# Optimization experiments

Hardware: AMD Instinct MI355X
Metric: run time of the kernel (lower is better)

Reference implementation:

```python
import jax, jax.numpy as jnp
import numpy as np

DIM = 1024
HEADS = 16
DIM_HEAD = 64
INNER = HEADS * DIM_HEAD  # 1024
EPS = 1e-5


def layernorm(x, w, b):
    mu = jnp.mean(x, axis=-1, keepdims=True)
    var = jnp.mean(jnp.square(x - mu), axis=-1, keepdims=True)
    return (x - mu) * jax.lax.rsqrt(var + EPS) * w + b


def setup_inputs() -> dict:
    key = jax.random.key(0)
    ks = jax.random.split(key, 9)
    b, n1, n2 = 4, 4096, 256
    x = jax.random.normal(ks[0], (b, n1, DIM), dtype=jnp.float32)
    latents = jax.random.normal(ks[1], (b, n2, DIM), dtype=jnp.float32)
    shift = jax.random.normal(ks[2], (b, HEADS), dtype=jnp.float32)
    scale = jax.random.normal(ks[3], (b, HEADS), dtype=jnp.float32)
    s = 1.0 / np.sqrt(DIM)
    Wq = jax.random.normal(ks[4], (DIM, INNER), dtype=jnp.float32) * s
    Wkv = jax.random.normal(ks[5], (DIM, 2 * INNER), dtype=jnp.float32) * s
    Wout = jax.random.normal(ks[6], (INNER, DIM), dtype=jnp.float32) * (1.0 / np.sqrt(INNER))
    ln1_w = jnp.ones((DIM,), jnp.float32)
    ln1_b = jnp.zeros((DIM,), jnp.float32)
    ln2_w = jnp.ones((DIM,), jnp.float32)
    ln2_b = jnp.zeros((DIM,), jnp.float32)
    return {"x": x, "latents": latents, "shift": shift, "scale": scale,
            "ln1_w": ln1_w, "ln1_b": ln1_b, "ln2_w": ln2_w, "ln2_b": ln2_b,
            "Wq": Wq, "Wkv": Wkv, "Wout": Wout}


def reference(x, latents, shift, scale, ln1_w, ln1_b, ln2_w, ln2_b, Wq, Wkv, Wout):
    b = x.shape[0]
    xn = layernorm(x, ln1_w, ln1_b)            # (b, n1, D)
    ln = layernorm(latents, ln2_w, ln2_b)      # (b, n2, D)
    q = ln @ Wq                                 # (b, n2, inner)
    kv = xn @ Wkv                               # (b, n1, 2*inner)
    k, v = jnp.split(kv, 2, axis=-1)
    q = q.reshape(b, -1, HEADS, DIM_HEAD)
    k = k.reshape(b, -1, HEADS, DIM_HEAD)
    v = v.reshape(b, -1, HEADS, DIM_HEAD)
    # AdaLN-style per-head modulation on q
    q = q * (1.0 + scale[:, None, :, None]) + shift[:, None, :, None]
    # fp32 attention scores (already fp32 here)
    attn_scale = DIM_HEAD ** -0.5
    qk = jnp.einsum('bihd,bjhd->bhij', q.astype(jnp.float32), k.astype(jnp.float32)) * attn_scale
    attn = jax.nn.softmax(qk, axis=-1).astype(v.dtype)  # (b, h, n2, n1)
    out = jnp.einsum('bhij,bjhd->bihd', attn, v)         # (b, n2, h, dh)
    out = out.reshape(b, -1, INNER)
    return out @ Wout
```

## Files before the change

### kernel.cpp

```cpp
#include <hip/hip_runtime.h>

typedef __bf16 bf16;
typedef bf16 bf16x8 __attribute__((ext_vector_type(8)));
typedef bf16 bf16x4 __attribute__((ext_vector_type(4)));
typedef float f32x4 __attribute__((ext_vector_type(4)));

#define B_ 4
#define N1 4096
#define N2 256
#define DIM 1024
#define HEADS 16
#define DH 64
#define INNER 1024
#define ASPLIT 4
#define KEYS_PER_SPLIT (N1 / ASPLIT)
#define SPLIT_ELEMS (4 * 16 * 256 * 64)
#define ROWS_TOTAL (4 * HEADS * N2)

typedef __attribute__((address_space(1))) const void gvoid_t;
typedef __attribute__((address_space(3))) void lvoid_t;
__device__ __forceinline__ void async16(const void* g, void* l) {
  __builtin_amdgcn_global_load_lds((gvoid_t*)g, (lvoid_t*)l, 16, 0, 0);
}

__global__ __launch_bounds__(256) void prep(
    const float* __restrict__ Wq, const float* __restrict__ Wkv,
    const float* __restrict__ Wout, bf16* __restrict__ WqT,
    bf16* __restrict__ WkvT, bf16* __restrict__ WoutT,
    const float* __restrict__ x, const float* __restrict__ latents,
    const float* __restrict__ ln1w, const float* __restrict__ ln1b,
    const float* __restrict__ ln2w, const float* __restrict__ ln2b,
    bf16* __restrict__ xn, bf16* __restrict__ lnl) {
  __shared__ float tile[32][33];
  int t = blockIdx.x;
  if (t < 4096) {
    const float* src;
    bf16* dst;
    int N;
    if (t < 1024) { src = Wq; dst = WqT; N = 1024; }
    else if (t < 3072) { t -= 1024; src = Wkv; dst = WkvT; N = 2048; }
    else { t -= 3072; src = Wout; dst = WoutT; N = 1024; }
    int ntiles = N >> 5;
    int n0 = (t % ntiles) * 32, k0 = (t / ntiles) * 32;
    int xx = threadIdx.x & 31, yy = threadIdx.x >> 5;
    for (int j = 0; j < 4; j++)
      tile[yy + 8 * j][xx] = src[(size_t)(k0 + yy + 8 * j) * N + n0 + xx];
    __syncthreads();
    for (int j = 0; j < 4; j++)
      dst[(size_t)(n0 + yy + 8 * j) * 1024 + k0 + xx] = (bf16)tile[xx][yy + 8 * j];
    return;
  }
  int wv = threadIdx.x >> 6, lane = threadIdx.x & 63;
  int grow = (t - 4096) * 4 + wv;
  const float *src, *w, *bb;
  bf16* dst;
  int row;
  if (grow < 16384) { src = x; w = ln1w; bb = ln1b; dst = xn; row = grow; }
  else { src = latents; w = ln2w; bb = ln2b; dst = lnl; row = grow - 16384; }
  const float4* p = (const float4*)(src + (size_t)row * DIM);
  float4 v[4];
  for (int j = 0; j < 4; j++) v[j] = p[j * 64 + lane];
  float s = 0.f, sq = 0.f;
  for (int j = 0; j < 4; j++) {
    s += v[j].x + v[j].y + v[j].z + v[j].w;
    sq += v[j].x * v[j].x + v[j].y * v[j].y + v[j].z * v[j].z + v[j].w * v[j].w;
  }
  for (int off = 32; off; off >>= 1) {
    s += __shfl_xor(s, off, 64);
    sq += __shfl_xor(sq, off, 64);
  }
  float mu = s * (1.0f / DIM);
  float var = sq * (1.0f / DIM) - mu * mu;
  float r = rsqrtf(var + 1e-5f);
  for (int j = 0; j < 4; j++) {
    float4 wv4 = ((const float4*)w)[j * 64 + lane];
    float4 bv4 = ((const float4*)bb)[j * 64 + lane];
    bf16x4 o;
    o[0] = (bf16)((v[j].x - mu) * r * wv4.x + bv4.x);
    o[1] = (bf16)((v[j].y - mu) * r * wv4.y + bv4.y);
    o[2] = (bf16)((v[j].z - mu) * r * wv4.z + bv4.z);
    o[3] = (bf16)((v[j].w - mu) * r * wv4.w + bv4.w);
    *(bf16x4*)(dst + (size_t)row * DIM + (j * 64 + lane) * 4) = o;
  }
}

__global__ __launch_bounds__(256) void gemm_kv(
    const bf16* __restrict__ A, const bf16* __restrict__ Bt,
    bf16* __restrict__ Cout, bf16* __restrict__ Cout2, int K) {
  __shared__ __align__(16) bf16 smem[128 * 64 * 2];
  bf16* As = smem;
  bf16* Bs = smem + 128 * 64;
  int tid = threadIdx.x;
  int lane = tid & 63, wv = tid >> 6;
  int wr = wv >> 1, wc = wv & 1;
  int quad = lane >> 4, lr = lane & 15;
  int bid = blockIdx.y * 16 + blockIdx.x;
  int c = bid & 7, g = bid >> 3;
  int mi = g & 7, nb = (g >> 3) & 15, chunk = g >> 7;
  int m0 = (chunk * 64 + mi * 8 + c) * 128;
  int n0 = nb * 128;
  f32x4 acc[4][4] = {};
  for (int kt = 0; kt < K; kt += 64) {
    __syncthreads();
    for (int j = 0; j < 4; j++) {
      int idx0 = j * 256 + wv * 64;
      int row = (idx0 >> 3) + (lane >> 3);
      int cb = (lane & 7) ^ (row & 7);
      async16(&A[(size_t)(m0 + row) * K + kt + cb * 8], &As[idx0 * 8]);
      async16(&Bt[(size_t)(n0 + row) * K + kt + cb * 8], &Bs[idx0 * 8]);
    }
    __syncthreads();
    for (int kk = 0; kk < 2; kk++) {
      bf16x8 af[4], bfr[4];
      for (int im = 0; im < 4; im++) {
        int row = wr * 64 + im * 16 + lr;
        af[im] = *(const bf16x8*)&As[row * 64 + ((quad + 4 * kk) ^ (row & 7)) * 8];
      }
      for (int in = 0; in < 4; in++) {
        int row = wc * 64 + in * 16 + lr;
        bfr[in] = *(const bf16x8*)&Bs[row * 64 + ((quad + 4 * kk) ^ (row & 7)) * 8];
      }
      for (int im = 0; im < 4; im++)
        for (int in = 0; in < 4; in++)
          acc[im][in] = __builtin_amdgcn_mfma_f32_16x16x32_bf16(
              af[im], bfr[in], acc[im][in], 0, 0, 0);
    }
  }

  if (n0 >= 1024) {
    bf16* Ct = smem;
    for (int pass = 0; pass < 2; pass++) {
      __syncthreads();
      for (int inL = 0; inL < 2; inL++) {
        int in = pass * 2 + inL;
        int cc = wc * 32 + inL * 16 + lr;
        for (int im = 0; im < 4; im++) {
          int rb = wr * 64 + im * 16 + quad * 4;
          bf16x4 pk;
          for (int r = 0; r < 4; r++) pk[r] = (bf16)acc[im][in][r];
          *(bf16x4*)&Ct[cc * 136 + rb] = pk;
        }
      }
      __syncthreads();
      for (int k2 = 0; k2 < 4; k2++) {
        int ci = k2 * 256 + tid;
        int cc = ci >> 4, ch = ci & 15;
        uint4 val = *(const uint4*)&Ct[cc * 136 + ch * 8];
        int gco = (cc >> 5) * 64 + pass * 32 + (cc & 31);
        int col = n0 - 1024 + gco;
        int bb2 = m0 >> 12;
        int key = (m0 & 4095) + ch * 8;
        *(uint4*)&Cout2[((size_t)(bb2 * 1024 + col)) * 4096 + key] = val;
      }
    }
    return;
  }

  for (int im = 0; im < 4; im++)
    for (int in = 0; in < 4; in++) {
      int col = n0 + wc * 64 + in * 16 + lr;
      for (int r = 0; r < 4; r++) {
        int row = m0 + wr * 64 + im * 16 + quad * 4 + r;
        Cout[(size_t)row * 1024 + col] = (bf16)acc[im][in][r];
      }
    }
}

template <int MODE>
__global__ __launch_bounds__(256) void gemm64(
    const bf16* __restrict__ A, const bf16* __restrict__ Bt,
    void* __restrict__ Cout, int K, int N,
    const float* __restrict__ shiftp, const float* __restrict__ scalep) {
  __shared__ __align__(16) bf16 As[64 * 64];
  __shared__ __align__(16) bf16 Bs[64 * 64];
  int tid = threadIdx.x;
  int lane = tid & 63, wv = tid >> 6;
  int wr = wv >> 1, wc = wv & 1;
  int quad = lane >> 4, lr = lane & 15;
  int m0 = blockIdx.y * 64, n0 = blockIdx.x * 64;
  f32x4 acc[2][2] = {};
  for (int kt = 0; kt < K; kt += 64) {
    __syncthreads();
    for (int j = 0; j < 2; j++) {
      int idx0 = j * 256 + wv * 64;
      int row = (idx0 >> 3) + (lane >> 3);
      int cb = (lane & 7) ^ (row & 7);
      async16(&A[(size_t)(m0 + row) * K + kt + cb * 8], &As[idx0 * 8]);
      async16(&Bt[(size_t)(n0 + row) * K + kt + cb * 8], &Bs[idx0 * 8]);
    }
    __syncthreads();
    for (int kk = 0; kk < 2; kk++) {
      bf16x8 af[2], bfr[2];
      for (int im = 0; im < 2; im++) {
        int row = wr * 32 + im * 16 + lr;
        af[im] = *(const bf16x8*)&As[row * 64 + ((quad + 4 * kk) ^ (row & 7)) * 8];
      }
      for (int in = 0; in < 2; in++) {
        int row = wc * 32 + in * 16 + lr;
        bfr[in] = *(const bf16x8*)&Bs[row * 64 + ((quad + 4 * kk) ^ (row & 7)) * 8];
      }
      for (int im = 0; im < 2; im++)
        for (int in = 0; in < 2; in++)
          acc[im][in] = __builtin_amdgcn_mfma_f32_16x16x32_bf16(
              af[im], bfr[in], acc[im][in], 0, 0, 0);
    }
  }
  for (int im = 0; im < 2; im++)
    for (int in = 0; in < 2; in++) {
      int col = n0 + wc * 32 + in * 16 + lr;
      for (int r = 0; r < 4; r++) {
        int row = m0 + wr * 32 + im * 16 + quad * 4 + r;
        float v = acc[im][in][r];
        if (MODE == 1) {
          int bb = row >> 8, hh = col >> 6;
          float sc = scalep[bb * 16 + hh], sh = shiftp[bb * 16 + hh];
          ((bf16*)Cout)[(size_t)row * N + col] =
              (bf16)((v * (1.0f + sc) + sh) * 0.18033688011112042f);
        } else {
          ((float*)Cout)[(size_t)row * N + col] = v;
        }
      }
    }
}

__global__ __launch_bounds__(256) void attn_kernel(const bf16* __restrict__ q,
                                                   const bf16* __restrict__ kb,
                                                   const bf16* __restrict__ vt,
                                                   bf16* __restrict__ opb,
                                                   float* __restrict__ lseb) {
  int b = blockIdx.z, h = blockIdx.y;
  int qp = blockIdx.x >> 2, sp = blockIdx.x & 3;
  int tid = threadIdx.x, lane = tid & 63, wv = tid >> 6;
  int quad = lane >> 4, lr = lane & 15;
  __shared__ __align__(16) bf16 Ks[64 * 64];
  __shared__ __align__(16) bf16 Vs[64 * 64];
  __shared__ __align__(16) bf16 QP[128 * 64];
  __shared__ float abuf[4][16];
  int q0 = qp * 128;

  const bf16* qg = q + (size_t)(b * N2 + q0) * INNER + h * DH;
  for (int j = 0; j < 4; j++) {
    int r0 = j * 32 + wv * 8;
    int r = r0 + (lane >> 3);
    async16(&qg[(size_t)r * INNER + ((lane & 7) ^ (r & 7)) * 8], &QP[r0 * 64]);
  }
  __syncthreads();
  bf16x8 aQ[2][2];
  for (int g = 0; g < 2; g++) {
    int row = wv * 32 + g * 16 + lr;
    for (int kk = 0; kk < 2; kk++)
      aQ[g][kk] = *(const bf16x8*)&QP[row * 64 + ((quad + 4 * kk) ^ (row & 7)) * 8];
  }
  float m_s[2] = {-1e30f, -1e30f}, l_s[2] = {0.0f, 0.0f};
  f32x4 oacc[2][4] = {};

  const bf16* kg = kb + (size_t)(b * N1) * 1024 + h * DH;
  const bf16* vg = vt + (size_t)((b * HEADS + h) * DH) * N1;
  bf16* Ps = QP + wv * 2048;

  for (int t = 0; t < KEYS_PER_SPLIT / 64; t++) {
    int key0 = sp * KEYS_PER_SPLIT + t * 64;
    __syncthreads();
    for (int j = 0; j < 2; j++) {
      int r0 = j * 32 + wv * 8;
      int r = r0 + (lane >> 3);
      int cs = ((lane & 7) ^ (r & 7)) * 8;
      async16(&kg[(size_t)(key0 + r) * 1024 + cs], &Ks[r0 * 64]);
      async16(&vg[(size_t)r * N1 + key0 + cs], &Vs[r0 * 64]);
    }
    __syncthreads();

    bf16x8 ak[2][4], bv[2][4];
    for (int kk = 0; kk < 2; kk++)
      for (int nt = 0; nt < 4; nt++) {
        int row = nt * 16 + lr;
        ak[kk][nt] =
            *(const bf16x8*)&Ks[row * 64 + ((quad + 4 * kk) ^ (row & 7)) * 8];
        bv[kk][nt] =
            *(const bf16x8*)&Vs[row * 64 + ((quad + 4 * kk) ^ (row & 7)) * 8];
      }

    for (int g = 0; g < 2; g++) {
      f32x4 s[4] = {};
      for (int kk = 0; kk < 2; kk++)
        for (int nt = 0; nt < 4; nt++)
          s[nt] = __builtin_amdgcn_mfma_f32_16x16x32_bf16(ak[kk][nt], aQ[g][kk],
                                                          s[nt], 0, 0, 0);
      float mx = s[0][0];
      for (int nt = 0; nt < 4; nt++)
        for (int r = 0; r < 4; r++) mx = fmaxf(mx, s[nt][r]);
      mx = fmaxf(mx, __shfl_xor(mx, 16, 64));
      mx = fmaxf(mx, __shfl_xor(mx, 32, 64));
      float mn = fmaxf(m_s[g], mx);
      float al = exp2f(m_s[g] - mn);
      float p[4][4], sum = 0.0f;
      for (int nt = 0; nt < 4; nt++)
        for (int r = 0; r < 4; r++) {
          p[nt][r] = exp2f(s[nt][r] - mn);
          sum += p[nt][r];
        }
      sum += __shfl_xor(sum, 16, 64);
      sum += __shfl_xor(sum, 32, 64);
      l_s[g] = l_s[g] * al + sum;
      m_s[g] = mn;
      if (quad == 0) abuf[wv][lr] = al;

      for (int nt = 0; nt < 4; nt++) {
        bf16x4 pk;
        for (int r = 0; r < 4; r++) pk[r] = (bf16)p[nt][r];
        *(bf16x4*)&Ps[lr * 64 + ((2 * nt + (quad >> 1)) ^ (lr & 7)) * 8 +
                      (quad & 1) * 4] = pk;
      }

      f32x4 a4 = *(const f32x4*)&abuf[wv][quad * 4];
      for (int in = 0; in < 4; in++)
        for (int r = 0; r < 4; r++) oacc[g][in][r] *= a4[r];

      bf16x8 aP[2];
      for (int kk = 0; kk < 2; kk++)
        aP[kk] = *(const bf16x8*)&Ps[lr * 64 + ((4 * kk + quad) ^ (lr & 7)) * 8];
      for (int kk = 0; kk < 2; kk++)
        for (int in = 0; in < 4; in++)
          oacc[g][in] = __builtin_amdgcn_mfma_f32_16x16x32_bf16(
              aP[kk], bv[kk][in], oacc[g][in], 0, 0, 0);
    }
  }

  bf16* ob = opb + (size_t)sp * SPLIT_ELEMS;
  size_t rbase = (size_t)(b * HEADS + h) * N2;
  for (int g = 0; g < 2; g++) {
    for (int r = 0; r < 4; r++) {
      float lrow = __shfl(l_s[g], quad * 4 + r, 16);
      float inv = 1.0f / lrow;
      int qq = q0 + wv * 32 + g * 16 + quad * 4 + r;
      for (int in = 0; in < 4; in++)
        ob[(rbase + qq) * 64 + in * 16 + lr] = (bf16)(oacc[g][in][r] * inv);
    }
    if (quad == 0) {
      int qq = q0 + wv * 32 + g * 16 + lr;
      lseb[(size_t)sp * ROWS_TOTAL + rbase + qq] = m_s[g] + __log2f(l_s[g]);
    }
  }
}

__global__ __launch_bounds__(256) void combine_kernel(const bf16* __restrict__ opb,
                                                      const float* __restrict__ lseb,
                                                      bf16* __restrict__ out) {
  int gid = blockIdx.x * 256 + threadIdx.x;
  int d = gid & 63;
  int rq = gid >> 6;
  int qq = rq & 255, bh = rq >> 8;
  int h = bh & 15, b = bh >> 4;
  float ls[ASPLIT];
  for (int s = 0; s < ASPLIT; s++) ls[s] = lseb[(size_t)s * ROWS_TOTAL + rq];
  float M = fmaxf(fmaxf(ls[0], ls[1]), fmaxf(ls[2], ls[3]));
  float L = 0.0f, o = 0.0f;
  for (int s = 0; s < ASPLIT; s++) {
    float w = exp2f(ls[s] - M);
    L += w;
    o += w * (float)opb[(size_t)s * SPLIT_ELEMS + (size_t)rq * 64 + d];
  }
  out[((size_t)(b * N2 + qq)) * INNER + h * DH + d] = (bf16)(o / L);
}

extern "C" void kernel_launch(void* const* d_in, const int* in_sizes, int n_in,
                              void* d_out, int out_size, void* d_ws,
                              size_t ws_size, hipStream_t stream) {
  const float* x       = (const float*)d_in[0];
  const float* latents = (const float*)d_in[1];
  const float* shift   = (const float*)d_in[2];
  const float* scale   = (const float*)d_in[3];
  const float* ln1w    = (const float*)d_in[4];
  const float* ln1b    = (const float*)d_in[5];
  const float* ln2w    = (const float*)d_in[6];
  const float* ln2b    = (const float*)d_in[7];
  const float* Wq      = (const float*)d_in[8];
  const float* Wkv     = (const float*)d_in[9];
  const float* Wout    = (const float*)d_in[10];

  char* ws = (char*)d_ws;
  bf16*  xn    = (bf16*)(ws);
  bf16*  opb   = (bf16*)(ws);
  bf16*  lnl   = (bf16*)(ws + 33554432);
  float* lseb  = (float*)(ws + 33554432);
  bf16*  qb    = (bf16*)(ws + 35651584);
  bf16*  kb    = (bf16*)(ws + 37748736);
  bf16*  vtb   = (bf16*)(ws + 104857600);
  bf16*  aob   = (bf16*)(ws + 138412032);
  bf16*  WqT   = (bf16*)(ws + 140509184);
  bf16*  WkvT  = (bf16*)(ws + 142606336);
  bf16*  WoutT = (bf16*)(ws + 146800640);

  prep<<<8448, 256, 0, stream>>>(Wq, Wkv, Wout, WqT, WkvT, WoutT, x, latents,
                                 ln1w, ln1b, ln2w, ln2b, xn, lnl);
  gemm_kv<<<dim3(16, 128), 256, 0, stream>>>(xn, WkvT, kb, vtb, 1024);
  gemm64<1><<<dim3(16, 16), 256, 0, stream>>>(lnl, WqT, qb, 1024, 1024, shift,
                                              scale);
  attn_kernel<<<dim3(2 * ASPLIT, 16, 4), 256, 0, stream>>>(qb, kb, vtb, opb,
                                                           lseb);
  combine_kernel<<<16384, 256, 0, stream>>>(opb, lseb, aob);
  gemm64<2><<<dim3(16, 16), 256, 0, stream>>>(aob, WoutT, d_out, 1024, 1024,
                                              nullptr, nullptr);
}
```

Measured before the change: 285.4 us.

## Rewrite KV GEMM with 256x256 tiles, double-buffered async LDS pipeline

```diff
diff --git a/kernel.cpp b/kernel.cpp
--- a/kernel.cpp
+++ b/kernel.cpp
@@ -84,86 +84,173 @@
   }
 }
 
-__global__ __launch_bounds__(256) void gemm_kv(
+__device__ __forceinline__ int swz_off(int row, int cb) {
+  int line = row >> 1;
+  return (line << 7) + (((((row & 1) << 2) | cb) ^ (line & 7)) << 4);
+}
+
+__global__ __launch_bounds__(512, 2) void gemm_kv256(
     const bf16* __restrict__ A, const bf16* __restrict__ Bt,
-    bf16* __restrict__ Cout, bf16* __restrict__ Cout2, int K) {
-  __shared__ __align__(16) bf16 smem[128 * 64 * 2];
-  bf16* As = smem;
-  bf16* Bs = smem + 128 * 64;
+    bf16* __restrict__ Cout, bf16* __restrict__ Cout2) {
+  extern __shared__ char smem[];
   int tid = threadIdx.x;
   int lane = tid & 63, wv = tid >> 6;
-  int wr = wv >> 1, wc = wv & 1;
-  int quad = lane >> 4, lr = lane & 15;
-  int bid = blockIdx.y * 16 + blockIdx.x;
-  int c = bid & 7, g = bid >> 3;
-  int mi = g & 7, nb = (g >> 3) & 15, chunk = g >> 7;
-  int m0 = (chunk * 64 + mi * 8 + c) * 128;
-  int n0 = nb * 128;
-  f32x4 acc[4][4] = {};
-  for (int kt = 0; kt < K; kt += 64) {
-    __syncthreads();
-    for (int j = 0; j < 4; j++) {
-      int idx0 = j * 256 + wv * 64;
-      int row = (idx0 >> 3) + (lane >> 3);
-      int cb = (lane & 7) ^ (row & 7);
-      async16(&A[(size_t)(m0 + row) * K + kt + cb * 8], &As[idx0 * 8]);
-      async16(&Bt[(size_t)(n0 + row) * K + kt + cb * 8], &Bs[idx0 * 8]);
-    }
-    __syncthreads();
-    for (int kk = 0; kk < 2; kk++) {
-      bf16x8 af[4], bfr[4];
-      for (int im = 0; im < 4; im++) {
-        int row = wr * 64 + im * 16 + lr;
-        af[im] = *(const bf16x8*)&As[row * 64 + ((quad + 4 * kk) ^ (row & 7)) * 8];
-      }
+  int lr = lane & 15, quad = lane >> 4;
+  int wr = wv >> 2, wc = wv & 3;
+  int bid = blockIdx.x;
+  int mt = (bid & 7) * 8 + ((bid >> 3) >> 3), nt = (bid >> 3) & 7;
+  int m0 = mt * 256, n0 = nt * 256;
+
+  int offA[8], offB[4];
+#pragma unroll
+  for (int im = 0; im < 8; im++) offA[im] = swz_off(wr * 128 + im * 16 + lr, quad);
+#pragma unroll
+  for (int in = 0; in < 4; in++) offB[in] = swz_off(wc * 64 + in * 16 + lr, quad);
+
+  size_t gA[2], gB[2];
+#pragma unroll
+  for (int s = 0; s < 2; s++) {
+    int u = s * 512 + tid;
+    int line = u >> 3, inner = (u & 7) ^ (line & 7);
+    int row = line * 2 + (inner >> 2), cb = inner & 3;
+    gA[s] = (size_t)(m0 + row) * 1024 + cb * 8;
+    gB[s] = (size_t)(n0 + row) * 1024 + cb * 8;
+  }
+  int ldsS0 = wv * 1024, ldsS1 = 8192 + wv * 1024;
+
+  auto stA = [&](int b, int kh, int k0) {
+    char* base = smem + b * 32768 + kh * 16384;
+    async16(&A[gA[0] + k0], base + ldsS0);
+    async16(&A[gA[1] + k0], base + ldsS1);
+  };
+  auto stB = [&](int b, int kh, int k0) {
+    char* base = smem + 65536 + b * 32768 + kh * 16384;
+    async16(&Bt[gB[0] + k0], base + ldsS0);
+    async16(&Bt[gB[1] + k0], base + ldsS1);
+  };
+
+  f32x4 acc[8][4] = {};
+
+  stA(0, 0, 0);  stB(0, 0, 0);
+  stA(0, 1, 32); stB(0, 1, 32);
+  stA(1, 0, 64); stB(1, 0, 64);
+  asm volatile("s_waitcnt vmcnt(4)" ::: "memory");
+  __builtin_amdgcn_s_barrier();
+
+#pragma unroll 1
+  for (int t = 0; t < 16; t++) {
+    int b = t & 1;
+    const char* A0 = smem + b * 32768;
+    const char* A1 = A0 + 16384;
+    const char* B0 = smem + 65536 + b * 32768;
+    const char* B1 = B0 + 16384;
+    int k1 = (t + 1 < 16 ? t + 1 : 15) * 64;
+    int k2 = (t + 2 < 16 ? t + 2 : 15) * 64;
+    bf16x8 af[4], bfr[4];
+#pragma unroll
+    for (int in = 0; in < 4; in++) bfr[in] = *(const bf16x8*)(B0 + offB[in]);
+#pragma unroll
+    for (int im = 0; im < 4; im++) af[im] = *(const bf16x8*)(A0 + offA[im]);
+    stA(b ^ 1, 1, k1 + 32);
+    __builtin_amdgcn_s_barrier();
+    __builtin_amdgcn_s_setprio(1);
+#pragma unroll
+    for (int im = 0; im < 4; im++)
+#pragma unroll
+      for (int in = 0; in < 4; in++)
+        acc[im][in] = __builtin_amdgcn_mfma_f32_16x16x32_bf16(
+            af[im], bfr[in], acc[im][in], 0, 0, 0);
+    __builtin_amdgcn_s_setprio(0);
+    __builtin_amdgcn_s_barrier();
+#pragma unroll
+    for (int im = 0; im < 4; im++) af[im] = *(const bf16x8*)(A0 + offA[4 + im]);
+    stB(b ^ 1, 1, k1 + 32);
+    __builtin_amdgcn_s_barrier();
+    __builtin_amdgcn_s_setprio(1);
+#pragma unroll
+    for (int im = 0; im < 4; im++)
+#pragma unroll
+      for (int in = 0; in < 4; in++)
+        acc[4 + im][in] = __builtin_amdgcn_mfma_f32_16x16x32_bf16(
+            af[im], bfr[in], acc[4 + im][in], 0, 0, 0);
+    __builtin_amdgcn_s_setprio(0);
+    __builtin_amdgcn_s_barrier();
+#pragma unroll
+    for (int in = 0; in < 4; in++) bfr[in] = *(const bf16x8*)(B1 + offB[in]);
+#pragma unroll
+    for (int im = 0; im < 4; im++) af[im] = *(const bf16x8*)(A1 + offA[im]);
+    stA(b, 0, k2);
+    __builtin_amdgcn_s_barrier();
+    __builtin_amdgcn_s_setprio(1);
+#pragma unroll
+    for (int im = 0; im < 4; im++)
+#pragma unroll
+      for (int in = 0; in < 4; in++)
+        acc[im][in] = __builtin_amdgcn_mfma_f32_16x16x32_bf16(
+            af[im], bfr[in], acc[im][in], 0, 0, 0);
+    __builtin_amdgcn_s_setprio(0);
+    __builtin_amdgcn_s_barrier();
+#pragma unroll
+    for (int im = 0; im < 4; im++) af[im] = *(const bf16x8*)(A1 + offA[4 + im]);
+    stB(b, 0, k2);
+    __builtin_amdgcn_s_barrier();
+    __builtin_amdgcn_s_setprio(1);
+#pragma unroll
+    for (int im = 0; im < 4; im++)
+#pragma unroll
+      for (int in = 0; in < 4; in++)
+        acc[4 + im][in] = __builtin_amdgcn_mfma_f32_16x16x32_bf16(
+            af[im], bfr[in], acc[4 + im][in], 0, 0, 0);
+    __builtin_amdgcn_s_setprio(0);
+    asm volatile("s_waitcnt vmcnt(4)" ::: "memory");
+    __builtin_amdgcn_s_barrier();
+  }
+
+  asm volatile("s_waitcnt vmcnt(0)" ::: "memory");
+  __builtin_amdgcn_s_barrier();
+
+  if (n0 < 1024) {
+#pragma unroll
+    for (int im = 0; im < 8; im++)
+#pragma unroll
       for (int in = 0; in < 4; in++) {
-        int row = wc * 64 + in * 16 + lr;
-        bfr[in] = *(const bf16x8*)&Bs[row * 64 + ((quad + 4 * kk) ^ (row & 7)) * 8];
-      }
-      for (int im = 0; im < 4; im++)
-        for (int in = 0; in < 4; in++)
-          acc[im][in] = __builtin_amdgcn_mfma_f32_16x16x32_bf16(
-              af[im], bfr[in], acc[im][in], 0, 0, 0);
-    }
-  }
-
-  if (n0 >= 1024) {
-    bf16* Ct = smem;
-    for (int pass = 0; pass < 2; pass++) {
-      __syncthreads();
-      for (int inL = 0; inL < 2; inL++) {
-        int in = pass * 2 + inL;
-        int cc = wc * 32 + inL * 16 + lr;
-        for (int im = 0; im < 4; im++) {
-          int rb = wr * 64 + im * 16 + quad * 4;
-          bf16x4 pk;
-          for (int r = 0; r < 4; r++) pk[r] = (bf16)acc[im][in][r];
-          *(bf16x4*)&Ct[cc * 136 + rb] = pk;
+        int col = n0 + wc * 64 + in * 16 + lr;
+#pragma unroll
+        for (int r = 0; r < 4; r++) {
+          int row = m0 + wr * 128 + im * 16 + quad * 4 + r;
+          Cout[(size_t)row * 1024 + col] = (bf16)acc[im][in][r];
         }
       }
-      __syncthreads();
-      for (int k2 = 0; k2 < 4; k2++) {
-        int ci = k2 * 256 + tid;
-        int cc = ci >> 4, ch = ci & 15;
-        uint4 val = *(const uint4*)&Ct[cc * 136 + ch * 8];
-        int gco = (cc >> 5) * 64 + pass * 32 + (cc & 31);
-        int col = n0 - 1024 + gco;
-        int bb2 = m0 >> 12;
-        int key = (m0 & 4095) + ch * 8;
-        *(uint4*)&Cout2[((size_t)(bb2 * 1024 + col)) * 4096 + key] = val;
-      }
-    }
     return;
   }
-
-  for (int im = 0; im < 4; im++)
-    for (int in = 0; in < 4; in++) {
-      int col = n0 + wc * 64 + in * 16 + lr;
-      for (int r = 0; r < 4; r++) {
-        int row = m0 + wr * 64 + im * 16 + quad * 4 + r;
-        Cout[(size_t)row * 1024 + col] = (bf16)acc[im][in][r];
-      }
-    }
+  int b2 = m0 >> 12;
+  int key0 = (m0 & 4095) + wr * 128;
+  int gc0 = (n0 - 1024) + wc * 64;
+  bf16* Tw = (bf16*)(smem + wv * 8704);
+  for (int pass = 0; pass < 2; pass++) {
+#pragma unroll
+    for (int ii = 0; ii < 2; ii++) {
+      int in = pass * 2 + ii;
+      int cl = ii * 16 + lr;
+#pragma unroll
+      for (int im = 0; im < 8; im++) {
+        bf16x4 pk;
+#pragma unroll
+        for (int r = 0; r < 4; r++) pk[r] = (bf16)acc[im][in][r];
+        *(bf16x4*)&Tw[cl * 136 + im * 16 + quad * 4] = pk;
+      }
+    }
+    asm volatile("s_waitcnt lgkmcnt(0)" ::: "memory");
+#pragma unroll
+    for (int j = 0; j < 8; j++) {
+      int idx = j * 64 + lane;
+      int cl = idx >> 4, k8 = idx & 15;
+      uint4 val = *(const uint4*)&Tw[cl * 136 + k8 * 8];
+      *(uint4*)&Cout2[((size_t)(b2 * 1024 + gc0 + pass * 32 + cl)) * 4096 +
+                      key0 + k8 * 8] = val;
+    }
+    asm volatile("s_waitcnt lgkmcnt(0)" ::: "memory");
+  }
 }
 
 template <int MODE>
@@ -391,9 +478,16 @@
   bf16*  WkvT  = (bf16*)(ws + 142606336);
   bf16*  WoutT = (bf16*)(ws + 146800640);
 
+  static bool attr_done = false;
+  if (!attr_done) {
+    hipFuncSetAttribute(reinterpret_cast<const void*>(gemm_kv256),
+                        hipFuncAttributeMaxDynamicSharedMemorySize, 131072);
+    attr_done = true;
+  }
+
   prep<<<8448, 256, 0, stream>>>(Wq, Wkv, Wout, WqT, WkvT, WoutT, x, latents,
                                  ln1w, ln1b, ln2w, ln2b, xn, lnl);
-  gemm_kv<<<dim3(16, 128), 256, 0, stream>>>(xn, WkvT, kb, vtb, 1024);
+  gemm_kv256<<<dim3(512), dim3(512), 131072, stream>>>(xn, WkvT, kb, vtb);
   gemm64<1><<<dim3(16, 16), 256, 0, stream>>>(lnl, WqT, qb, 1024, 1024, shift,
                                               scale);
   attn_kernel<<<dim3(2 * ASPLIT, 16, 4), 256, 0, stream>>>(qb, kb, vtb, opb,
```

Result: faster. 275.8 us (-3.4%).
